# Kernel optimization log

Measured on AMD Instinct MI355X. Metric: run time of the kernel, lower is better.

Reference implementation:

```python
import jax, jax.numpy as jnp
import numpy as np

C_EMB = 64  # n_embd


def setup_inputs() -> dict:
    key = jax.random.key(0)
    ks = jax.random.split(key, 7)
    B, T, C, H, BS = 2, 512, C_EMB, 64, 512
    s = lambda k, shp, sc: (jax.random.normal(k, shp, dtype=jnp.float32) * sc)
    return {
        "x": s(ks[0], (B, T, C), 1.0),
        "pos_table": s(ks[1], (BS, C), 0.02),
        "W1": s(ks[2], (C, 4 * C), (4 * C) ** -0.5),  # Linear(4C -> C), torch layout [out,in]
        "b1": s(ks[3], (C,), 0.01),
        "W2": s(ks[4], (1, C), C ** -0.5),            # Linear(C -> 1)
        "b2": s(ks[5], (1,), 0.01),
        "Wv": s(ks[6], (H, C), C ** -0.5),            # Linear(C -> H, bias=False)
    }


def reference(x, pos_table, W1, b1, W2, b2, Wv):
    B, T, C = x.shape
    # x1 = cat([pos_emb, x], -1): [B,T,2C]
    pos = pos_table[:T]  # [T,C]
    x1 = jnp.concatenate([jnp.broadcast_to(pos[None], (B, T, C)), x], axis=-1)  # [B,T,2C]
    # a2[b,i,j] = cat([x1[b,j], x1[b,i]]); Linear(4C->C) splits into key/query halves.
    Wk = W1[:, : 2 * C]   # acts on x1_j
    Wq = W1[:, 2 * C :]   # acts on x1_i
    hk = jnp.einsum('btd,cd->btc', x1, Wk)  # [B,T,C] indexed by j
    hq = jnp.einsum('btd,cd->btc', x1, Wq)  # [B,T,C] indexed by i
    hidden = jax.nn.relu(hq[:, :, None, :] + hk[:, None, :, :] + b1)  # [B,T(i),T(j),C]
    scores = jnp.einsum('bijc,c->bij', hidden, W2[0]) + b2[0]          # [B,T,T]
    wei = scores * (C ** -0.5)
    causal = jnp.tril(jnp.ones((T, T), dtype=bool))
    wei = jnp.where(causal[None], wei, -jnp.inf)
    wei = jax.nn.softmax(wei, axis=-1)  # dropout p=0 -> identity
    v = jnp.einsum('btc,hc->bth', x, Wv)  # [B,T,H]
    return jnp.einsum('bij,bjh->bih', wei, v)
```

## Files before the change

### kernel.cpp

```cpp
#include <hip/hip_runtime.h>
#include <math.h>

constexpr int TLEN = 512;
constexpr int CDIM = 64;
constexpr int BDIM = 2;

__global__ __launch_bounds__(512) void hk_kernel(
    const float* __restrict__ x, const float* __restrict__ pos,
    const float* __restrict__ W1, float4* __restrict__ hkt4)
{
    const int tid = threadIdx.x;
    const int r0g = blockIdx.x * 8;
    const int b   = r0g >> 9;
    const int t0  = r0g & (TLEN - 1);

    __shared__ float4 wk_s[64 * 32];
    __shared__ alignas(16) float x1s[8][128];
    __shared__ float hks[CDIM][9];

    const float4* W1f4 = (const float4*)W1;
    #pragma unroll
    for (int m = tid; m < 64 * 32; m += 512) {
        const int c = m >> 5, e4 = m & 31;
        wk_s[c * 32 + (e4 ^ (c & 31))] = W1f4[c * 64 + e4];
    }
    #pragma unroll
    for (int e = tid; e < 8 * 128; e += 512) {
        const int r4 = e >> 7, d = e & 127;
        const int grow = r0g + r4;
        const int tt = grow & (TLEN - 1);
        x1s[r4][d] = (d < CDIM) ? pos[tt * CDIM + d]
                                : x[grow * CDIM + (d - CDIM)];
    }
    __syncthreads();

    {
        const int sub = tid >> 6, c = tid & 63;
        const float4* xv = (const float4*)x1s[sub];
        const float4* wb = wk_s + c * 32;
        const int sw = c & 31;
        float4 a = make_float4(0.f, 0.f, 0.f, 0.f);
        #pragma unroll
        for (int d4 = 0; d4 < 32; ++d4) {
            const float4 xx = xv[d4];
            const float4 ww = wb[d4 ^ sw];
            a.x = fmaf(xx.x, ww.x, a.x); a.y = fmaf(xx.y, ww.y, a.y);
            a.z = fmaf(xx.z, ww.z, a.z); a.w = fmaf(xx.w, ww.w, a.w);
        }
        hks[c][sub] = (a.x + a.y) + (a.z + a.w);
    }
    __syncthreads();

    if (tid < 128) {
        const int c4 = tid >> 3, tl = tid & 7;
        const float4 v = make_float4(hks[c4 * 4 + 0][tl], hks[c4 * 4 + 1][tl],
                                     hks[c4 * 4 + 2][tl], hks[c4 * 4 + 3][tl]);
        hkt4[(b * 16 + c4) * TLEN + t0 + tl] = v;
    }
}

__global__ __launch_bounds__(512) void attn_kernel(
    const float* __restrict__ x,  const float* __restrict__ pos,
    const float* __restrict__ W1, const float* __restrict__ b1,
    const float* __restrict__ W2, const float* __restrict__ b2,
    const float* __restrict__ Wv, const float4* __restrict__ hkt4,
    float* __restrict__ out)
{
    const int tid = threadIdx.x;
    const int idx = blockIdx.x;
    const int b   = idx & 1;
    const int p   = idx >> 1;
    int r[4];
    r[0] = p; r[1] = p + 128; r[2] = 383 - p; r[3] = 511 - p;

    __shared__ float4 wq_s[64 * 32];
    __shared__ float4 wv_s[64 * 16];
    __shared__ alignas(16) float x1s[4][128];
    __shared__ float hqp[4][CDIM][2];
    __shared__ alignas(16) float hq_sf[4][CDIM];
    __shared__ float4 w24_s[16];
    __shared__ alignas(16) float pS[4][TLEN];
    __shared__ float4 wredm[8];
    __shared__ float4 wreds[8];
    __shared__ float pvs[4][8][CDIM];
    __shared__ alignas(16) float o_s[4][CDIM];

    const float4* W1f4 = (const float4*)W1;
    #pragma unroll
    for (int m = tid; m < 64 * 32; m += 512) {
        const int c = m >> 5, e4 = m & 31;
        wq_s[c * 32 + (e4 ^ (c & 31))] = W1f4[c * 64 + 32 + e4];
    }
    const float4* Wvf4 = (const float4*)Wv;
    #pragma unroll
    for (int m = tid; m < 64 * 16; m += 512) {
        const int hh = m >> 4, e4 = m & 15;
        wv_s[hh * 16 + (e4 ^ (hh & 15))] = Wvf4[hh * 16 + e4];
    }
    {
        const int rp = tid >> 7, d = tid & 127;
        const int i  = r[rp];
        x1s[rp][d] = (d < CDIM) ? pos[i * CDIM + d]
                                : x[(b * TLEN + i) * CDIM + (d - CDIM)];
        if (tid < 16) w24_s[tid] = ((const float4*)W2)[tid];
    }
    __syncthreads();

    {
        const int k = tid >> 7, part = (tid >> 6) & 1, c = tid & 63;
        const float4* xv = ((const float4*)x1s[k]) + part * 16;
        const float4* wb = wq_s + c * 32;
        const int sw = c & 31;
        float4 a = make_float4(0.f, 0.f, 0.f, 0.f);
        #pragma unroll
        for (int d4 = 0; d4 < 16; ++d4) {
            const float4 xx = xv[d4];
            const float4 ww = wb[(part * 16 + d4) ^ sw];
            a.x = fmaf(xx.x, ww.x, a.x); a.y = fmaf(xx.y, ww.y, a.y);
            a.z = fmaf(xx.z, ww.z, a.z); a.w = fmaf(xx.w, ww.w, a.w);
        }
        hqp[k][c][part] = (a.x + a.y) + (a.z + a.w);
    }
    __syncthreads();
    if (tid < 256) {
        const int k = tid >> 6, c = tid & 63;
        hq_sf[k][c] = hqp[k][c][0] + hqp[k][c][1] + b1[c];
    }
    __syncthreads();

    const float b2v = b2[0];
    const float4* hk4b = hkt4 + b * 16 * TLEN;
    const int j = tid;

    float4 acc0 = make_float4(0.f, 0.f, 0.f, 0.f);
    float4 acc1 = acc0, acc2 = acc0, acc3 = acc0;
    #pragma unroll
    for (int c4 = 0; c4 < 16; ++c4) {
        const float4 kk = hk4b[c4 * TLEN + j];
        const float4 ww = w24_s[c4];
        const float4 q0 = ((const float4*)hq_sf[0])[c4];
        const float4 q1 = ((const float4*)hq_sf[1])[c4];
        const float4 q2 = ((const float4*)hq_sf[2])[c4];
        const float4 q3 = ((const float4*)hq_sf[3])[c4];
        acc0.x = fmaf(fmaxf(kk.x + q0.x, 0.f), ww.x, acc0.x);
        acc0.y = fmaf(fmaxf(kk.y + q0.y, 0.f), ww.y, acc0.y);
        acc0.z = fmaf(fmaxf(kk.z + q0.z, 0.f), ww.z, acc0.z);
        acc0.w = fmaf(fmaxf(kk.w + q0.w, 0.f), ww.w, acc0.w);
        acc1.x = fmaf(fmaxf(kk.x + q1.x, 0.f), ww.x, acc1.x);
        acc1.y = fmaf(fmaxf(kk.y + q1.y, 0.f), ww.y, acc1.y);
        acc1.z = fmaf(fmaxf(kk.z + q1.z, 0.f), ww.z, acc1.z);
        acc1.w = fmaf(fmaxf(kk.w + q1.w, 0.f), ww.w, acc1.w);
        acc2.x = fmaf(fmaxf(kk.x + q2.x, 0.f), ww.x, acc2.x);
        acc2.y = fmaf(fmaxf(kk.y + q2.y, 0.f), ww.y, acc2.y);
        acc2.z = fmaf(fmaxf(kk.z + q2.z, 0.f), ww.z, acc2.z);
        acc2.w = fmaf(fmaxf(kk.w + q2.w, 0.f), ww.w, acc2.w);
        acc3.x = fmaf(fmaxf(kk.x + q3.x, 0.f), ww.x, acc3.x);
        acc3.y = fmaf(fmaxf(kk.y + q3.y, 0.f), ww.y, acc3.y);
        acc3.z = fmaf(fmaxf(kk.z + q3.z, 0.f), ww.z, acc3.z);
        acc3.w = fmaf(fmaxf(kk.w + q3.w, 0.f), ww.w, acc3.w);
    }
    float s[4];
    s[0] = (acc0.x + acc0.y) + (acc0.z + acc0.w);
    s[1] = (acc1.x + acc1.y) + (acc1.z + acc1.w);
    s[2] = (acc2.x + acc2.y) + (acc2.z + acc2.w);
    s[3] = (acc3.x + acc3.y) + (acc3.z + acc3.w);
    bool valid[4];
    float mw[4], pt[4], sw2[4];
    #pragma unroll
    for (int k = 0; k < 4; ++k) {
        valid[k] = (j <= r[k]);
        s[k] = valid[k] ? (s[k] + b2v) * 0.125f : -1e30f;
        float m = s[k];
        #pragma unroll
        for (int off = 32; off > 0; off >>= 1)
            m = fmaxf(m, __shfl_xor(m, off));
        mw[k] = m;
        pt[k] = valid[k] ? __expf(s[k] - m) : 0.f;
        float sm = pt[k];
        #pragma unroll
        for (int off = 32; off > 0; off >>= 1)
            sm += __shfl_xor(sm, off);
        sw2[k] = sm;
    }
    const int w = tid >> 6;
    if ((tid & 63) == 0) {
        wredm[w] = make_float4(mw[0], mw[1], mw[2], mw[3]);
        wreds[w] = make_float4(sw2[0], sw2[1], sw2[2], sw2[3]);
    }
    __syncthreads();

    float4 gm = wredm[0];
    #pragma unroll
    for (int ww = 1; ww < 8; ++ww) {
        const float4 rm = wredm[ww];
        gm.x = fmaxf(gm.x, rm.x); gm.y = fmaxf(gm.y, rm.y);
        gm.z = fmaxf(gm.z, rm.z); gm.w = fmaxf(gm.w, rm.w);
    }
    float4 gs = make_float4(0.f, 0.f, 0.f, 0.f);
    #pragma unroll
    for (int ww = 0; ww < 8; ++ww) {
        const float4 rm = wredm[ww];
        const float4 rs = wreds[ww];
        gs.x = fmaf(rs.x, __expf(rm.x - gm.x), gs.x);
        gs.y = fmaf(rs.y, __expf(rm.y - gm.y), gs.y);
        gs.z = fmaf(rs.z, __expf(rm.z - gm.z), gs.z);
        gs.w = fmaf(rs.w, __expf(rm.w - gm.w), gs.w);
    }
    const float* gmp = (const float*)&gm;
    const float* gsp = (const float*)&gs;
    #pragma unroll
    for (int k = 0; k < 4; ++k)
        pS[k][j] = pt[k] * (__expf(mw[k] - gmp[k]) / gsp[k]);
    __syncthreads();

    const int h = tid & 63;
    const int g = w;
    const float* xh = x + b * TLEN * CDIM + h;
    const int nj4 = (r[3] >> 2) + 1;
    float4 a0 = make_float4(0.f, 0.f, 0.f, 0.f);
    float4 a1 = a0, a2 = a0, a3 = a0;
    for (int j4 = g; j4 < nj4; j4 += 8) {
        const float4 p0 = ((const float4*)pS[0])[j4];
        const float4 p1 = ((const float4*)pS[1])[j4];
        const float4 p2 = ((const float4*)pS[2])[j4];
        const float4 p3 = ((const float4*)pS[3])[j4];
        const int j0 = j4 * 4;
        const float x0 = xh[j0 * CDIM];
        const float x1 = xh[(j0 + 1) * CDIM];
        const float x2 = xh[(j0 + 2) * CDIM];
        const float x3 = xh[(j0 + 3) * CDIM];
        a0.x = fmaf(p0.x, x0, a0.x); a0.y = fmaf(p0.y, x1, a0.y);
        a0.z = fmaf(p0.z, x2, a0.z); a0.w = fmaf(p0.w, x3, a0.w);
        a1.x = fmaf(p1.x, x0, a1.x); a1.y = fmaf(p1.y, x1, a1.y);
        a1.z = fmaf(p1.z, x2, a1.z); a1.w = fmaf(p1.w, x3, a1.w);
        a2.x = fmaf(p2.x, x0, a2.x); a2.y = fmaf(p2.y, x1, a2.y);
        a2.z = fmaf(p2.z, x2, a2.z); a2.w = fmaf(p2.w, x3, a2.w);
        a3.x = fmaf(p3.x, x0, a3.x); a3.y = fmaf(p3.y, x1, a3.y);
        a3.z = fmaf(p3.z, x2, a3.z); a3.w = fmaf(p3.w, x3, a3.w);
    }
    pvs[0][g][h] = (a0.x + a0.y) + (a0.z + a0.w);
    pvs[1][g][h] = (a1.x + a1.y) + (a1.z + a1.w);
    pvs[2][g][h] = (a2.x + a2.y) + (a2.z + a2.w);
    pvs[3][g][h] = (a3.x + a3.y) + (a3.z + a3.w);
    __syncthreads();
    if (tid < 256) {
        const int k = tid >> 6, hh = tid & 63;
        float o = pvs[k][0][hh];
        #pragma unroll
        for (int ww = 1; ww < 8; ++ww) o += pvs[k][ww][hh];
        o_s[k][hh] = o;
    }
    __syncthreads();
    if (tid < 256) {
        const int k = tid >> 6, hh = tid & 63;
        const float4* wb = wv_s + hh * 16;
        const int sw = hh & 15;
        const float4* o4 = (const float4*)o_s[k];
        float4 a = make_float4(0.f, 0.f, 0.f, 0.f);
        #pragma unroll
        for (int c4 = 0; c4 < 16; ++c4) {
            const float4 wwv = wb[c4 ^ sw];
            const float4 oo = o4[c4];
            a.x = fmaf(oo.x, wwv.x, a.x); a.y = fmaf(oo.y, wwv.y, a.y);
            a.z = fmaf(oo.z, wwv.z, a.z); a.w = fmaf(oo.w, wwv.w, a.w);
        }
        out[(b * TLEN + r[k]) * CDIM + hh] = (a.x + a.y) + (a.z + a.w);
    }
}

extern "C" void kernel_launch(void* const* d_in, const int* in_sizes, int n_in,
                              void* d_out, int out_size, void* d_ws, size_t ws_size,
                              hipStream_t stream)
{
    const float* x   = (const float*)d_in[0];
    const float* pos = (const float*)d_in[1];
    const float* W1  = (const float*)d_in[2];
    const float* b1  = (const float*)d_in[3];
    const float* W2  = (const float*)d_in[4];
    const float* b2  = (const float*)d_in[5];
    const float* Wv  = (const float*)d_in[6];
    float* out = (float*)d_out;

    float4* hkt4 = (float4*)d_ws;

    hk_kernel<<<BDIM * TLEN / 8, 512, 0, stream>>>(x, pos, W1, hkt4);
    attn_kernel<<<BDIM * TLEN / 4, 512, 0, stream>>>(x, pos, W1, b1, W2, b2, Wv,
                                                     hkt4, out);
}
```

Before: 21.15 us.

## Halve rows per attention block and skip fully-masked causal warps

The attention kernel now handles two paired rows (p and 511-p) per block instead of four, doubling the grid, and the hk kernel processes four rows per 256-thread block. Score computation is skipped for warps whose key range lies entirely beyond the query row, and the PV accumulation for the short row stops at its causal bound. The aim is to raise parallelism and cut wasted masked work, at the cost of reloading the Wq and Wv weights into shared memory in twice as many blocks.

After: 20.46 us. -3.3%, faster.

```diff
diff --git a/kernel.cpp b/kernel.cpp
--- a/kernel.cpp
+++ b/kernel.cpp
@@ -5,27 +5,27 @@
 constexpr int CDIM = 64;
 constexpr int BDIM = 2;
 
-__global__ __launch_bounds__(512) void hk_kernel(
+__global__ __launch_bounds__(256) void hk_kernel(
     const float* __restrict__ x, const float* __restrict__ pos,
     const float* __restrict__ W1, float4* __restrict__ hkt4)
 {
     const int tid = threadIdx.x;
-    const int r0g = blockIdx.x * 8;
+    const int r0g = blockIdx.x * 4;
     const int b   = r0g >> 9;
     const int t0  = r0g & (TLEN - 1);
 
     __shared__ float4 wk_s[64 * 32];
-    __shared__ alignas(16) float x1s[8][128];
-    __shared__ float hks[CDIM][9];
+    __shared__ alignas(16) float x1s[4][128];
+    __shared__ float hks[CDIM][5];
 
     const float4* W1f4 = (const float4*)W1;
     #pragma unroll
-    for (int m = tid; m < 64 * 32; m += 512) {
+    for (int m = tid; m < 64 * 32; m += 256) {
         const int c = m >> 5, e4 = m & 31;
         wk_s[c * 32 + (e4 ^ (c & 31))] = W1f4[c * 64 + e4];
     }
     #pragma unroll
-    for (int e = tid; e < 8 * 128; e += 512) {
+    for (int e = tid; e < 4 * 128; e += 256) {
         const int r4 = e >> 7, d = e & 127;
         const int grow = r0g + r4;
         const int tt = grow & (TLEN - 1);
@@ -51,15 +51,15 @@
     }
     __syncthreads();
 
-    if (tid < 128) {
-        const int c4 = tid >> 3, tl = tid & 7;
+    if (tid < 64) {
+        const int c4 = tid >> 2, tl = tid & 3;
         const float4 v = make_float4(hks[c4 * 4 + 0][tl], hks[c4 * 4 + 1][tl],
                                      hks[c4 * 4 + 2][tl], hks[c4 * 4 + 3][tl]);
         hkt4[(b * 16 + c4) * TLEN + t0 + tl] = v;
     }
 }
 
-__global__ __launch_bounds__(512) void attn_kernel(
+__global__ __launch_bounds__(512, 4) void attn_kernel(
     const float* __restrict__ x,  const float* __restrict__ pos,
     const float* __restrict__ W1, const float* __restrict__ b1,
     const float* __restrict__ W2, const float* __restrict__ b2,
@@ -70,20 +70,20 @@
     const int idx = blockIdx.x;
     const int b   = idx & 1;
     const int p   = idx >> 1;
-    int r[4];
-    r[0] = p; r[1] = p + 128; r[2] = 383 - p; r[3] = 511 - p;
+    int rr[2];
+    rr[0] = p; rr[1] = (TLEN - 1) - p;
 
     __shared__ float4 wq_s[64 * 32];
     __shared__ float4 wv_s[64 * 16];
-    __shared__ alignas(16) float x1s[4][128];
-    __shared__ float hqp[4][CDIM][2];
-    __shared__ alignas(16) float hq_sf[4][CDIM];
+    __shared__ alignas(16) float x1s[2][128];
+    __shared__ float hqp[2][CDIM][4];
+    __shared__ alignas(16) float hq_sf[2][CDIM];
     __shared__ float4 w24_s[16];
-    __shared__ alignas(16) float pS[4][TLEN];
-    __shared__ float4 wredm[8];
-    __shared__ float4 wreds[8];
-    __shared__ float pvs[4][8][CDIM];
-    __shared__ alignas(16) float o_s[4][CDIM];
+    __shared__ alignas(16) float pS[2][TLEN];
+    __shared__ float2 wredm[8];
+    __shared__ float2 wreds[8];
+    __shared__ float pvs[2][8][CDIM];
+    __shared__ alignas(16) float o_s[2][CDIM];
 
     const float4* W1f4 = (const float4*)W1;
     #pragma unroll
@@ -97,153 +97,130 @@
         const int hh = m >> 4, e4 = m & 15;
         wv_s[hh * 16 + (e4 ^ (hh & 15))] = Wvf4[hh * 16 + e4];
     }
-    {
+    if (tid < 256) {
         const int rp = tid >> 7, d = tid & 127;
-        const int i  = r[rp];
+        const int i  = rr[rp];
         x1s[rp][d] = (d < CDIM) ? pos[i * CDIM + d]
                                 : x[(b * TLEN + i) * CDIM + (d - CDIM)];
-        if (tid < 16) w24_s[tid] = ((const float4*)W2)[tid];
+    } else if (tid < 272) {
+        w24_s[tid - 256] = ((const float4*)W2)[tid - 256];
     }
     __syncthreads();
 
     {
-        const int k = tid >> 7, part = (tid >> 6) & 1, c = tid & 63;
-        const float4* xv = ((const float4*)x1s[k]) + part * 16;
+        const int k = tid >> 8, part = (tid >> 6) & 3, c = tid & 63;
+        const float4* xv = ((const float4*)x1s[k]) + part * 8;
         const float4* wb = wq_s + c * 32;
         const int sw = c & 31;
         float4 a = make_float4(0.f, 0.f, 0.f, 0.f);
         #pragma unroll
-        for (int d4 = 0; d4 < 16; ++d4) {
+        for (int d4 = 0; d4 < 8; ++d4) {
             const float4 xx = xv[d4];
-            const float4 ww = wb[(part * 16 + d4) ^ sw];
+            const float4 ww = wb[(part * 8 + d4) ^ sw];
             a.x = fmaf(xx.x, ww.x, a.x); a.y = fmaf(xx.y, ww.y, a.y);
             a.z = fmaf(xx.z, ww.z, a.z); a.w = fmaf(xx.w, ww.w, a.w);
         }
         hqp[k][c][part] = (a.x + a.y) + (a.z + a.w);
     }
     __syncthreads();
-    if (tid < 256) {
+    if (tid < 128) {
         const int k = tid >> 6, c = tid & 63;
-        hq_sf[k][c] = hqp[k][c][0] + hqp[k][c][1] + b1[c];
+        hq_sf[k][c] = hqp[k][c][0] + hqp[k][c][1] + hqp[k][c][2]
+                    + hqp[k][c][3] + b1[c];
     }
     __syncthreads();
 
     const float b2v = b2[0];
     const float4* hk4b = hkt4 + b * 16 * TLEN;
     const int j = tid;
-
-    float4 acc0 = make_float4(0.f, 0.f, 0.f, 0.f);
-    float4 acc1 = acc0, acc2 = acc0, acc3 = acc0;
-    #pragma unroll
-    for (int c4 = 0; c4 < 16; ++c4) {
-        const float4 kk = hk4b[c4 * TLEN + j];
-        const float4 ww = w24_s[c4];
-        const float4 q0 = ((const float4*)hq_sf[0])[c4];
-        const float4 q1 = ((const float4*)hq_sf[1])[c4];
-        const float4 q2 = ((const float4*)hq_sf[2])[c4];
-        const float4 q3 = ((const float4*)hq_sf[3])[c4];
-        acc0.x = fmaf(fmaxf(kk.x + q0.x, 0.f), ww.x, acc0.x);
-        acc0.y = fmaf(fmaxf(kk.y + q0.y, 0.f), ww.y, acc0.y);
-        acc0.z = fmaf(fmaxf(kk.z + q0.z, 0.f), ww.z, acc0.z);
-        acc0.w = fmaf(fmaxf(kk.w + q0.w, 0.f), ww.w, acc0.w);
-        acc1.x = fmaf(fmaxf(kk.x + q1.x, 0.f), ww.x, acc1.x);
-        acc1.y = fmaf(fmaxf(kk.y + q1.y, 0.f), ww.y, acc1.y);
-        acc1.z = fmaf(fmaxf(kk.z + q1.z, 0.f), ww.z, acc1.z);
-        acc1.w = fmaf(fmaxf(kk.w + q1.w, 0.f), ww.w, acc1.w);
-        acc2.x = fmaf(fmaxf(kk.x + q2.x, 0.f), ww.x, acc2.x);
-        acc2.y = fmaf(fmaxf(kk.y + q2.y, 0.f), ww.y, acc2.y);
-        acc2.z = fmaf(fmaxf(kk.z + q2.z, 0.f), ww.z, acc2.z);
-        acc2.w = fmaf(fmaxf(kk.w + q2.w, 0.f), ww.w, acc2.w);
-        acc3.x = fmaf(fmaxf(kk.x + q3.x, 0.f), ww.x, acc3.x);
-        acc3.y = fmaf(fmaxf(kk.y + q3.y, 0.f), ww.y, acc3.y);
-        acc3.z = fmaf(fmaxf(kk.z + q3.z, 0.f), ww.z, acc3.z);
-        acc3.w = fmaf(fmaxf(kk.w + q3.w, 0.f), ww.w, acc3.w);
-    }
-    float s[4];
-    s[0] = (acc0.x + acc0.y) + (acc0.z + acc0.w);
-    s[1] = (acc1.x + acc1.y) + (acc1.z + acc1.w);
-    s[2] = (acc2.x + acc2.y) + (acc2.z + acc2.w);
-    s[3] = (acc3.x + acc3.y) + (acc3.z + acc3.w);
-    bool valid[4];
-    float mw[4], pt[4], sw2[4];
-    #pragma unroll
-    for (int k = 0; k < 4; ++k) {
-        valid[k] = (j <= r[k]);
-        s[k] = valid[k] ? (s[k] + b2v) * 0.125f : -1e30f;
-        float m = s[k];
-        #pragma unroll
-        for (int off = 32; off > 0; off >>= 1)
-            m = fmaxf(m, __shfl_xor(m, off));
-        mw[k] = m;
-        pt[k] = valid[k] ? __expf(s[k] - m) : 0.f;
-        float sm = pt[k];
-        #pragma unroll
-        for (int off = 32; off > 0; off >>= 1)
-            sm += __shfl_xor(sm, off);
-        sw2[k] = sm;
-    }
     const int w = tid >> 6;
+
+    float mw[2], pt[2], swv[2];
+    #pragma unroll
+    for (int k = 0; k < 2; ++k) {
+        const int rk = rr[k];
+        if ((w << 6) <= rk) {
+            const float4* hq4 = (const float4*)hq_sf[k];
+            float4 acc = make_float4(0.f, 0.f, 0.f, 0.f);
+            #pragma unroll
+            for (int c4 = 0; c4 < 16; ++c4) {
+                const float4 kk = hk4b[c4 * TLEN + j];
+                const float4 qq = hq4[c4];
+                const float4 w2v = w24_s[c4];
+                acc.x = fmaf(fmaxf(kk.x + qq.x, 0.f), w2v.x, acc.x);
+                acc.y = fmaf(fmaxf(kk.y + qq.y, 0.f), w2v.y, acc.y);
+                acc.z = fmaf(fmaxf(kk.z + qq.z, 0.f), w2v.z, acc.z);
+                acc.w = fmaf(fmaxf(kk.w + qq.w, 0.f), w2v.w, acc.w);
+            }
+            const bool vld = (j <= rk);
+            const float sv = vld ? ((acc.x + acc.y) + (acc.z + acc.w) + b2v)
+                                   * 0.125f
+                                 : -1e30f;
+            float m = sv;
+            #pragma unroll
+            for (int off = 32; off > 0; off >>= 1)
+                m = fmaxf(m, __shfl_xor(m, off));
+            mw[k] = m;
+            pt[k] = vld ? __expf(sv - m) : 0.f;
+            float sm = pt[k];
+            #pragma unroll
+            for (int off = 32; off > 0; off >>= 1)
+                sm += __shfl_xor(sm, off);
+            swv[k] = sm;
+        } else {
+            mw[k] = -1e30f; pt[k] = 0.f; swv[k] = 0.f;
+        }
+    }
     if ((tid & 63) == 0) {
-        wredm[w] = make_float4(mw[0], mw[1], mw[2], mw[3]);
-        wreds[w] = make_float4(sw2[0], sw2[1], sw2[2], sw2[3]);
-    }
-    __syncthreads();
-
-    float4 gm = wredm[0];
-    #pragma unroll
-    for (int ww = 1; ww < 8; ++ww) {
-        const float4 rm = wredm[ww];
-        gm.x = fmaxf(gm.x, rm.x); gm.y = fmaxf(gm.y, rm.y);
-        gm.z = fmaxf(gm.z, rm.z); gm.w = fmaxf(gm.w, rm.w);
-    }
-    float4 gs = make_float4(0.f, 0.f, 0.f, 0.f);
+        wredm[w] = make_float2(mw[0], mw[1]);
+        wreds[w] = make_float2(swv[0], swv[1]);
+    }
+    __syncthreads();
+
+    float gm0 = -1e30f, gm1 = -1e30f;
     #pragma unroll
     for (int ww = 0; ww < 8; ++ww) {
-        const float4 rm = wredm[ww];
-        const float4 rs = wreds[ww];
-        gs.x = fmaf(rs.x, __expf(rm.x - gm.x), gs.x);
-        gs.y = fmaf(rs.y, __expf(rm.y - gm.y), gs.y);
-        gs.z = fmaf(rs.z, __expf(rm.z - gm.z), gs.z);
-        gs.w = fmaf(rs.w, __expf(rm.w - gm.w), gs.w);
-    }
-    const float* gmp = (const float*)&gm;
-    const float* gsp = (const float*)&gs;
-    #pragma unroll
-    for (int k = 0; k < 4; ++k)
-        pS[k][j] = pt[k] * (__expf(mw[k] - gmp[k]) / gsp[k]);
+        const float2 rm = wredm[ww];
+        gm0 = fmaxf(gm0, rm.x);
+        gm1 = fmaxf(gm1, rm.y);
+    }
+    float gs0 = 0.f, gs1 = 0.f;
+    #pragma unroll
+    for (int ww = 0; ww < 8; ++ww) {
+        const float2 rm = wredm[ww];
+        const float2 rs = wreds[ww];
+        gs0 = fmaf(rs.x, __expf(rm.x - gm0), gs0);
+        gs1 = fmaf(rs.y, __expf(rm.y - gm1), gs1);
+    }
+    pS[0][j] = pt[0] * (__expf(mw[0] - gm0) / gs0);
+    pS[1][j] = pt[1] * (__expf(mw[1] - gm1) / gs1);
     __syncthreads();
 
     const int h = tid & 63;
     const int g = w;
     const float* xh = x + b * TLEN * CDIM + h;
-    const int nj4 = (r[3] >> 2) + 1;
+    const int nj4 = (rr[1] >> 2) + 1;
     float4 a0 = make_float4(0.f, 0.f, 0.f, 0.f);
-    float4 a1 = a0, a2 = a0, a3 = a0;
+    float4 a1 = a0;
     for (int j4 = g; j4 < nj4; j4 += 8) {
-        const float4 p0 = ((const float4*)pS[0])[j4];
-        const float4 p1 = ((const float4*)pS[1])[j4];
-        const float4 p2 = ((const float4*)pS[2])[j4];
-        const float4 p3 = ((const float4*)pS[3])[j4];
         const int j0 = j4 * 4;
+        const float4 p1v = ((const float4*)pS[1])[j4];
         const float x0 = xh[j0 * CDIM];
         const float x1 = xh[(j0 + 1) * CDIM];
         const float x2 = xh[(j0 + 2) * CDIM];
         const float x3 = xh[(j0 + 3) * CDIM];
-        a0.x = fmaf(p0.x, x0, a0.x); a0.y = fmaf(p0.y, x1, a0.y);
-        a0.z = fmaf(p0.z, x2, a0.z); a0.w = fmaf(p0.w, x3, a0.w);
-        a1.x = fmaf(p1.x, x0, a1.x); a1.y = fmaf(p1.y, x1, a1.y);
-        a1.z = fmaf(p1.z, x2, a1.z); a1.w = fmaf(p1.w, x3, a1.w);
-        a2.x = fmaf(p2.x, x0, a2.x); a2.y = fmaf(p2.y, x1, a2.y);
-        a2.z = fmaf(p2.z, x2, a2.z); a2.w = fmaf(p2.w, x3, a2.w);
-        a3.x = fmaf(p3.x, x0, a3.x); a3.y = fmaf(p3.y, x1, a3.y);
-        a3.z = fmaf(p3.z, x2, a3.z); a3.w = fmaf(p3.w, x3, a3.w);
+        a1.x = fmaf(p1v.x, x0, a1.x); a1.y = fmaf(p1v.y, x1, a1.y);
+        a1.z = fmaf(p1v.z, x2, a1.z); a1.w = fmaf(p1v.w, x3, a1.w);
+        if (j0 <= rr[0]) {
+            const float4 p0v = ((const float4*)pS[0])[j4];
+            a0.x = fmaf(p0v.x, x0, a0.x); a0.y = fmaf(p0v.y, x1, a0.y);
+            a0.z = fmaf(p0v.z, x2, a0.z); a0.w = fmaf(p0v.w, x3, a0.w);
+        }
     }
     pvs[0][g][h] = (a0.x + a0.y) + (a0.z + a0.w);
     pvs[1][g][h] = (a1.x + a1.y) + (a1.z + a1.w);
-    pvs[2][g][h] = (a2.x + a2.y) + (a2.z + a2.w);
-    pvs[3][g][h] = (a3.x + a3.y) + (a3.z + a3.w);
-    __syncthreads();
-    if (tid < 256) {
+    __syncthreads();
+    if (tid < 128) {
         const int k = tid >> 6, hh = tid & 63;
         float o = pvs[k][0][hh];
         #pragma unroll
@@ -251,7 +228,7 @@
         o_s[k][hh] = o;
     }
     __syncthreads();
-    if (tid < 256) {
+    if (tid < 128) {
         const int k = tid >> 6, hh = tid & 63;
         const float4* wb = wv_s + hh * 16;
         const int sw = hh & 15;
@@ -264,7 +241,7 @@
             a.x = fmaf(oo.x, wwv.x, a.x); a.y = fmaf(oo.y, wwv.y, a.y);
             a.z = fmaf(oo.z, wwv.z, a.z); a.w = fmaf(oo.w, wwv.w, a.w);
         }
-        out[(b * TLEN + r[k]) * CDIM + hh] = (a.x + a.y) + (a.z + a.w);
+        out[(b * TLEN + rr[k]) * CDIM + hh] = (a.x + a.y) + (a.z + a.w);
     }
 }
 
@@ -283,7 +260,7 @@
 
     float4* hkt4 = (float4*)d_ws;
 
-    hk_kernel<<<BDIM * TLEN / 8, 512, 0, stream>>>(x, pos, W1, hkt4);
-    attn_kernel<<<BDIM * TLEN / 4, 512, 0, stream>>>(x, pos, W1, b1, W2, b2, Wv,
+    hk_kernel<<<BDIM * TLEN / 4, 256, 0, stream>>>(x, pos, W1, hkt4);
+    attn_kernel<<<BDIM * TLEN / 2, 512, 0, stream>>>(x, pos, W1, b1, W2, b2, Wv,
                                                      hkt4, out);
 }
```

## Precompute query projection in first kernel and skip fully masked causal work

Applied to the files above, without the earlier changes.

The projection kernel now computes both the key and query halves of the first linear layer (with bias) for every row and writes the query projection to workspace. The attention kernel no longer loads W1 into shared memory or recomputes queries per block, and reads W2 and the query rows directly from global memory. It also skips score, softmax and PV accumulation for wavefronts and j ranges lying entirely above the causal boundary of each query row. In exchange it adds an extra global round trip for the queries and introduces divergent branches in the inner loops.

New measurement: 25.89 us. +22.4%, slower.

```diff
diff --git a/kernel.cpp b/kernel.cpp
--- a/kernel.cpp
+++ b/kernel.cpp
@@ -5,27 +5,28 @@
 constexpr int CDIM = 64;
 constexpr int BDIM = 2;
 
-__global__ __launch_bounds__(512) void hk_kernel(
+__global__ __launch_bounds__(256) void proj_kernel(
     const float* __restrict__ x, const float* __restrict__ pos,
-    const float* __restrict__ W1, float4* __restrict__ hkt4)
+    const float* __restrict__ W1, const float* __restrict__ b1,
+    float4* __restrict__ hkt4, float* __restrict__ hqb)
 {
     const int tid = threadIdx.x;
-    const int r0g = blockIdx.x * 8;
+    const int r0g = blockIdx.x * 4;
     const int b   = r0g >> 9;
     const int t0  = r0g & (TLEN - 1);
 
-    __shared__ float4 wk_s[64 * 32];
-    __shared__ alignas(16) float x1s[8][128];
-    __shared__ float hks[CDIM][9];
+    __shared__ float4 w1_s[64 * 64];
+    __shared__ alignas(16) float x1s[4][128];
+    __shared__ float hks[CDIM][5];
 
     const float4* W1f4 = (const float4*)W1;
     #pragma unroll
-    for (int m = tid; m < 64 * 32; m += 512) {
-        const int c = m >> 5, e4 = m & 31;
-        wk_s[c * 32 + (e4 ^ (c & 31))] = W1f4[c * 64 + e4];
-    }
-    #pragma unroll
-    for (int e = tid; e < 8 * 128; e += 512) {
+    for (int m = tid; m < 64 * 64; m += 256) {
+        const int c = m >> 6, e4 = m & 63;
+        w1_s[c * 64 + (e4 ^ (c & 63))] = W1f4[c * 64 + e4];
+    }
+    #pragma unroll
+    for (int e = tid; e < 4 * 128; e += 256) {
         const int r4 = e >> 7, d = e & 127;
         const int grow = r0g + r4;
         const int tt = grow & (TLEN - 1);
@@ -36,23 +37,29 @@
 
     {
         const int sub = tid >> 6, c = tid & 63;
+        const int grow = r0g + sub;
         const float4* xv = (const float4*)x1s[sub];
-        const float4* wb = wk_s + c * 32;
-        const int sw = c & 31;
-        float4 a = make_float4(0.f, 0.f, 0.f, 0.f);
+        const float4* wb = w1_s + c * 64;
+        const int sw = c & 63;
+        float4 ak = make_float4(0.f, 0.f, 0.f, 0.f);
+        float4 aq = ak;
         #pragma unroll
         for (int d4 = 0; d4 < 32; ++d4) {
             const float4 xx = xv[d4];
-            const float4 ww = wb[d4 ^ sw];
-            a.x = fmaf(xx.x, ww.x, a.x); a.y = fmaf(xx.y, ww.y, a.y);
-            a.z = fmaf(xx.z, ww.z, a.z); a.w = fmaf(xx.w, ww.w, a.w);
-        }
-        hks[c][sub] = (a.x + a.y) + (a.z + a.w);
-    }
-    __syncthreads();
-
-    if (tid < 128) {
-        const int c4 = tid >> 3, tl = tid & 7;
+            const float4 wk = wb[d4 ^ sw];
+            const float4 wq = wb[(32 + d4) ^ sw];
+            ak.x = fmaf(xx.x, wk.x, ak.x); ak.y = fmaf(xx.y, wk.y, ak.y);
+            ak.z = fmaf(xx.z, wk.z, ak.z); ak.w = fmaf(xx.w, wk.w, ak.w);
+            aq.x = fmaf(xx.x, wq.x, aq.x); aq.y = fmaf(xx.y, wq.y, aq.y);
+            aq.z = fmaf(xx.z, wq.z, aq.z); aq.w = fmaf(xx.w, wq.w, aq.w);
+        }
+        hks[c][sub] = (ak.x + ak.y) + (ak.z + ak.w);
+        hqb[grow * CDIM + c] = (aq.x + aq.y) + (aq.z + aq.w) + b1[c];
+    }
+    __syncthreads();
+
+    if (tid < 64) {
+        const int c4 = tid >> 2, tl = tid & 3;
         const float4 v = make_float4(hks[c4 * 4 + 0][tl], hks[c4 * 4 + 1][tl],
                                      hks[c4 * 4 + 2][tl], hks[c4 * 4 + 3][tl]);
         hkt4[(b * 16 + c4) * TLEN + t0 + tl] = v;
@@ -60,10 +67,9 @@
 }
 
 __global__ __launch_bounds__(512) void attn_kernel(
-    const float* __restrict__ x,  const float* __restrict__ pos,
-    const float* __restrict__ W1, const float* __restrict__ b1,
-    const float* __restrict__ W2, const float* __restrict__ b2,
-    const float* __restrict__ Wv, const float4* __restrict__ hkt4,
+    const float* __restrict__ x,   const float* __restrict__ W2,
+    const float* __restrict__ b2,  const float* __restrict__ Wv,
+    const float4* __restrict__ hkt4, const float4* __restrict__ hqb4,
     float* __restrict__ out)
 {
     const int tid = threadIdx.x;
@@ -73,116 +79,98 @@
     int r[4];
     r[0] = p; r[1] = p + 128; r[2] = 383 - p; r[3] = 511 - p;
 
-    __shared__ float4 wq_s[64 * 32];
     __shared__ float4 wv_s[64 * 16];
-    __shared__ alignas(16) float x1s[4][128];
-    __shared__ float hqp[4][CDIM][2];
-    __shared__ alignas(16) float hq_sf[4][CDIM];
-    __shared__ float4 w24_s[16];
     __shared__ alignas(16) float pS[4][TLEN];
     __shared__ float4 wredm[8];
     __shared__ float4 wreds[8];
     __shared__ float pvs[4][8][CDIM];
     __shared__ alignas(16) float o_s[4][CDIM];
 
-    const float4* W1f4 = (const float4*)W1;
-    #pragma unroll
-    for (int m = tid; m < 64 * 32; m += 512) {
-        const int c = m >> 5, e4 = m & 31;
-        wq_s[c * 32 + (e4 ^ (c & 31))] = W1f4[c * 64 + 32 + e4];
-    }
     const float4* Wvf4 = (const float4*)Wv;
     #pragma unroll
     for (int m = tid; m < 64 * 16; m += 512) {
         const int hh = m >> 4, e4 = m & 15;
         wv_s[hh * 16 + (e4 ^ (hh & 15))] = Wvf4[hh * 16 + e4];
     }
-    {
-        const int rp = tid >> 7, d = tid & 127;
-        const int i  = r[rp];
-        x1s[rp][d] = (d < CDIM) ? pos[i * CDIM + d]
-                                : x[(b * TLEN + i) * CDIM + (d - CDIM)];
-        if (tid < 16) w24_s[tid] = ((const float4*)W2)[tid];
-    }
-    __syncthreads();
-
-    {
-        const int k = tid >> 7, part = (tid >> 6) & 1, c = tid & 63;
-        const float4* xv = ((const float4*)x1s[k]) + part * 16;
-        const float4* wb = wq_s + c * 32;
-        const int sw = c & 31;
-        float4 a = make_float4(0.f, 0.f, 0.f, 0.f);
-        #pragma unroll
-        for (int d4 = 0; d4 < 16; ++d4) {
-            const float4 xx = xv[d4];
-            const float4 ww = wb[(part * 16 + d4) ^ sw];
-            a.x = fmaf(xx.x, ww.x, a.x); a.y = fmaf(xx.y, ww.y, a.y);
-            a.z = fmaf(xx.z, ww.z, a.z); a.w = fmaf(xx.w, ww.w, a.w);
-        }
-        hqp[k][c][part] = (a.x + a.y) + (a.z + a.w);
-    }
-    __syncthreads();
-    if (tid < 256) {
-        const int k = tid >> 6, c = tid & 63;
-        hq_sf[k][c] = hqp[k][c][0] + hqp[k][c][1] + b1[c];
-    }
-    __syncthreads();
 
     const float b2v = b2[0];
     const float4* hk4b = hkt4 + b * 16 * TLEN;
+    const float4* W2f4 = (const float4*)W2;
+    const float4* q0p = hqb4 + (b * TLEN + r[0]) * 16;
+    const float4* q1p = hqb4 + (b * TLEN + r[1]) * 16;
+    const float4* q2p = hqb4 + (b * TLEN + r[2]) * 16;
+    const float4* q3p = hqb4 + (b * TLEN + r[3]) * 16;
+
     const int j = tid;
+    const int w = tid >> 6;
+    const int wbase = w << 6;
+    const bool act0 = (wbase <= r[0]);
+    const bool act1 = (wbase <= r[1]);
+    const bool act2 = (wbase <= r[2]);
 
     float4 acc0 = make_float4(0.f, 0.f, 0.f, 0.f);
     float4 acc1 = acc0, acc2 = acc0, acc3 = acc0;
     #pragma unroll
     for (int c4 = 0; c4 < 16; ++c4) {
         const float4 kk = hk4b[c4 * TLEN + j];
-        const float4 ww = w24_s[c4];
-        const float4 q0 = ((const float4*)hq_sf[0])[c4];
-        const float4 q1 = ((const float4*)hq_sf[1])[c4];
-        const float4 q2 = ((const float4*)hq_sf[2])[c4];
-        const float4 q3 = ((const float4*)hq_sf[3])[c4];
-        acc0.x = fmaf(fmaxf(kk.x + q0.x, 0.f), ww.x, acc0.x);
-        acc0.y = fmaf(fmaxf(kk.y + q0.y, 0.f), ww.y, acc0.y);
-        acc0.z = fmaf(fmaxf(kk.z + q0.z, 0.f), ww.z, acc0.z);
-        acc0.w = fmaf(fmaxf(kk.w + q0.w, 0.f), ww.w, acc0.w);
-        acc1.x = fmaf(fmaxf(kk.x + q1.x, 0.f), ww.x, acc1.x);
-        acc1.y = fmaf(fmaxf(kk.y + q1.y, 0.f), ww.y, acc1.y);
-        acc1.z = fmaf(fmaxf(kk.z + q1.z, 0.f), ww.z, acc1.z);
-        acc1.w = fmaf(fmaxf(kk.w + q1.w, 0.f), ww.w, acc1.w);
-        acc2.x = fmaf(fmaxf(kk.x + q2.x, 0.f), ww.x, acc2.x);
-        acc2.y = fmaf(fmaxf(kk.y + q2.y, 0.f), ww.y, acc2.y);
-        acc2.z = fmaf(fmaxf(kk.z + q2.z, 0.f), ww.z, acc2.z);
-        acc2.w = fmaf(fmaxf(kk.w + q2.w, 0.f), ww.w, acc2.w);
-        acc3.x = fmaf(fmaxf(kk.x + q3.x, 0.f), ww.x, acc3.x);
-        acc3.y = fmaf(fmaxf(kk.y + q3.y, 0.f), ww.y, acc3.y);
-        acc3.z = fmaf(fmaxf(kk.z + q3.z, 0.f), ww.z, acc3.z);
-        acc3.w = fmaf(fmaxf(kk.w + q3.w, 0.f), ww.w, acc3.w);
-    }
+        const float4 ww = W2f4[c4];
+        if (act0) {
+            const float4 qq = q0p[c4];
+            acc0.x = fmaf(fmaxf(kk.x + qq.x, 0.f), ww.x, acc0.x);
+            acc0.y = fmaf(fmaxf(kk.y + qq.y, 0.f), ww.y, acc0.y);
+            acc0.z = fmaf(fmaxf(kk.z + qq.z, 0.f), ww.z, acc0.z);
+            acc0.w = fmaf(fmaxf(kk.w + qq.w, 0.f), ww.w, acc0.w);
+        }
+        if (act1) {
+            const float4 qq = q1p[c4];
+            acc1.x = fmaf(fmaxf(kk.x + qq.x, 0.f), ww.x, acc1.x);
+            acc1.y = fmaf(fmaxf(kk.y + qq.y, 0.f), ww.y, acc1.y);
+            acc1.z = fmaf(fmaxf(kk.z + qq.z, 0.f), ww.z, acc1.z);
+            acc1.w = fmaf(fmaxf(kk.w + qq.w, 0.f), ww.w, acc1.w);
+        }
+        if (act2) {
+            const float4 qq = q2p[c4];
+            acc2.x = fmaf(fmaxf(kk.x + qq.x, 0.f), ww.x, acc2.x);
+            acc2.y = fmaf(fmaxf(kk.y + qq.y, 0.f), ww.y, acc2.y);
+            acc2.z = fmaf(fmaxf(kk.z + qq.z, 0.f), ww.z, acc2.z);
+            acc2.w = fmaf(fmaxf(kk.w + qq.w, 0.f), ww.w, acc2.w);
+        }
+        {
+            const float4 qq = q3p[c4];
+            acc3.x = fmaf(fmaxf(kk.x + qq.x, 0.f), ww.x, acc3.x);
+            acc3.y = fmaf(fmaxf(kk.y + qq.y, 0.f), ww.y, acc3.y);
+            acc3.z = fmaf(fmaxf(kk.z + qq.z, 0.f), ww.z, acc3.z);
+            acc3.w = fmaf(fmaxf(kk.w + qq.w, 0.f), ww.w, acc3.w);
+        }
+    }
+
     float s[4];
     s[0] = (acc0.x + acc0.y) + (acc0.z + acc0.w);
     s[1] = (acc1.x + acc1.y) + (acc1.z + acc1.w);
     s[2] = (acc2.x + acc2.y) + (acc2.z + acc2.w);
     s[3] = (acc3.x + acc3.y) + (acc3.z + acc3.w);
-    bool valid[4];
+    const bool act[4] = { act0, act1, act2, true };
     float mw[4], pt[4], sw2[4];
     #pragma unroll
     for (int k = 0; k < 4; ++k) {
-        valid[k] = (j <= r[k]);
-        s[k] = valid[k] ? (s[k] + b2v) * 0.125f : -1e30f;
-        float m = s[k];
-        #pragma unroll
-        for (int off = 32; off > 0; off >>= 1)
-            m = fmaxf(m, __shfl_xor(m, off));
-        mw[k] = m;
-        pt[k] = valid[k] ? __expf(s[k] - m) : 0.f;
-        float sm = pt[k];
-        #pragma unroll
-        for (int off = 32; off > 0; off >>= 1)
-            sm += __shfl_xor(sm, off);
-        sw2[k] = sm;
-    }
-    const int w = tid >> 6;
+        if (act[k]) {
+            const bool vld = (j <= r[k]);
+            const float sv = vld ? (s[k] + b2v) * 0.125f : -1e30f;
+            float m = sv;
+            #pragma unroll
+            for (int off = 32; off > 0; off >>= 1)
+                m = fmaxf(m, __shfl_xor(m, off));
+            mw[k] = m;
+            pt[k] = vld ? __expf(sv - m) : 0.f;
+            float sm = pt[k];
+            #pragma unroll
+            for (int off = 32; off > 0; off >>= 1)
+                sm += __shfl_xor(sm, off);
+            sw2[k] = sm;
+        } else {
+            mw[k] = -1e30f; pt[k] = 0.f; sw2[k] = 0.f;
+        }
+    }
     if ((tid & 63) == 0) {
         wredm[w] = make_float4(mw[0], mw[1], mw[2], mw[3]);
         wreds[w] = make_float4(sw2[0], sw2[1], sw2[2], sw2[3]);
@@ -220,23 +208,29 @@
     float4 a0 = make_float4(0.f, 0.f, 0.f, 0.f);
     float4 a1 = a0, a2 = a0, a3 = a0;
     for (int j4 = g; j4 < nj4; j4 += 8) {
-        const float4 p0 = ((const float4*)pS[0])[j4];
-        const float4 p1 = ((const float4*)pS[1])[j4];
-        const float4 p2 = ((const float4*)pS[2])[j4];
-        const float4 p3 = ((const float4*)pS[3])[j4];
         const int j0 = j4 * 4;
+        const float4 p3v = ((const float4*)pS[3])[j4];
         const float x0 = xh[j0 * CDIM];
         const float x1 = xh[(j0 + 1) * CDIM];
         const float x2 = xh[(j0 + 2) * CDIM];
         const float x3 = xh[(j0 + 3) * CDIM];
-        a0.x = fmaf(p0.x, x0, a0.x); a0.y = fmaf(p0.y, x1, a0.y);
-        a0.z = fmaf(p0.z, x2, a0.z); a0.w = fmaf(p0.w, x3, a0.w);
-        a1.x = fmaf(p1.x, x0, a1.x); a1.y = fmaf(p1.y, x1, a1.y);
-        a1.z = fmaf(p1.z, x2, a1.z); a1.w = fmaf(p1.w, x3, a1.w);
-        a2.x = fmaf(p2.x, x0, a2.x); a2.y = fmaf(p2.y, x1, a2.y);
-        a2.z = fmaf(p2.z, x2, a2.z); a2.w = fmaf(p2.w, x3, a2.w);
-        a3.x = fmaf(p3.x, x0, a3.x); a3.y = fmaf(p3.y, x1, a3.y);
-        a3.z = fmaf(p3.z, x2, a3.z); a3.w = fmaf(p3.w, x3, a3.w);
+        a3.x = fmaf(p3v.x, x0, a3.x); a3.y = fmaf(p3v.y, x1, a3.y);
+        a3.z = fmaf(p3v.z, x2, a3.z); a3.w = fmaf(p3v.w, x3, a3.w);
+        if (j0 <= r[2]) {
+            const float4 pv = ((const float4*)pS[2])[j4];
+            a2.x = fmaf(pv.x, x0, a2.x); a2.y = fmaf(pv.y, x1, a2.y);
+            a2.z = fmaf(pv.z, x2, a2.z); a2.w = fmaf(pv.w, x3, a2.w);
+        }
+        if (j0 <= r[1]) {
+            const float4 pv = ((const float4*)pS[1])[j4];
+            a1.x = fmaf(pv.x, x0, a1.x); a1.y = fmaf(pv.y, x1, a1.y);
+            a1.z = fmaf(pv.z, x2, a1.z); a1.w = fmaf(pv.w, x3, a1.w);
+        }
+        if (j0 <= r[0]) {
+            const float4 pv = ((const float4*)pS[0])[j4];
+            a0.x = fmaf(pv.x, x0, a0.x); a0.y = fmaf(pv.y, x1, a0.y);
+            a0.z = fmaf(pv.z, x2, a0.z); a0.w = fmaf(pv.w, x3, a0.w);
+        }
     }
     pvs[0][g][h] = (a0.x + a0.y) + (a0.z + a0.w);
     pvs[1][g][h] = (a1.x + a1.y) + (a1.z + a1.w);
@@ -282,8 +276,10 @@
     float* out = (float*)d_out;
 
     float4* hkt4 = (float4*)d_ws;
-
-    hk_kernel<<<BDIM * TLEN / 8, 512, 0, stream>>>(x, pos, W1, hkt4);
-    attn_kernel<<<BDIM * TLEN / 4, 512, 0, stream>>>(x, pos, W1, b1, W2, b2, Wv,
-                                                     hkt4, out);
+    float*  hqb  = (float*)d_ws + 4 * 16384;
+
+    proj_kernel<<<BDIM * TLEN / 4, 256, 0, stream>>>(x, pos, W1, b1, hkt4, hqb);
+    attn_kernel<<<BDIM * TLEN / 4, 512, 0, stream>>>(x, W2, b2, Wv,
+                                                     hkt4, (const float4*)hqb,
+                                                     out);
 }
```
